# Kernel tuning notes

Measured on AMD Instinct MI355X. Metric: run time of the kernel, lower is better.

Reference implementation:

```python
import jax, jax.numpy as jnp
import numpy as np
from jax import lax

D_MODEL = 1024
D_IN = 1024        # expand=1 -> d_inner = d_model
N_STATE = 16       # d_state
DT_RANK = 64       # ceil(d_model/16)
D_FFN = 4096
BATCH, SEQ = 2, 2048


def setup_inputs() -> dict:
    key = jax.random.key(0)
    ks = jax.random.split(key, 12)
    r = lambda i, shape, s=0.02: jax.random.normal(ks[i], shape, jnp.float32) * s
    ones = lambda n: jnp.ones((n,), jnp.float32)
    zeros = lambda n: jnp.zeros((n,), jnp.float32)
    # S4D-real init for A
    A_log = jnp.log(jnp.tile(jnp.arange(1, N_STATE + 1, dtype=jnp.float32), (D_IN, 1)))
    return {
        "src": jax.random.normal(ks[0], (BATCH, SEQ, D_MODEL), jnp.float32),
        "in_proj_w": r(1, (2 * D_IN, D_MODEL)),
        "conv_w": r(2, (D_IN, 2), 0.5),
        "conv_b": zeros(D_IN),
        "x_proj_w": r(3, (DT_RANK + 2 * N_STATE, D_IN)),
        "dt_proj_w": r(4, (D_IN, DT_RANK), 0.1),
        "dt_proj_b": r(5, (D_IN,), 0.1),
        "A_log": A_log,
        "Dp": ones(D_IN),
        "out_proj_w": r(6, (D_MODEL, D_IN)),
        "mnorm_g": ones(D_MODEL), "mnorm_b": zeros(D_MODEL),
        "n1_g": ones(D_MODEL), "n1_b": zeros(D_MODEL),
        "n2_g": ones(D_MODEL), "n2_b": zeros(D_MODEL),
        "n3_g": ones(D_MODEL), "n3_b": zeros(D_MODEL),
        "ffn_w1": r(7, (D_FFN, D_MODEL)),
        "ffn_w2": r(8, (D_MODEL, D_FFN)),
        "fe_w": r(9, (D_MODEL, D_MODEL)),
        "fe_b": zeros(D_MODEL),
    }


def _ln(x, g, b, eps=1e-5):
    m = x.mean(-1, keepdims=True)
    v = ((x - m) ** 2).mean(-1, keepdims=True)
    return (x - m) / jnp.sqrt(v + eps) * g + b


def _mamba(x, in_proj_w, conv_w, conv_b, x_proj_w, dt_proj_w, dt_proj_b,
           A_log, Dp, out_proj_w):
    B, L, _ = x.shape
    xz = x @ in_proj_w.T                       # (B,L,2*D_IN)
    x_in, z = jnp.split(xz, 2, axis=-1)
    # depthwise causal conv1d, kernel size 2: y[l] = w0*x[l-1] + w1*x[l] + b
    x_prev = jnp.pad(x_in, ((0, 0), (1, 0), (0, 0)))[:, :L]
    x_c = jax.nn.silu(x_prev * conv_w[:, 0] + x_in * conv_w[:, 1] + conv_b)
    x_dbl = x_c @ x_proj_w.T                   # (B,L,DT_RANK+2N)
    dt, Bm, Cm = jnp.split(x_dbl, [DT_RANK, DT_RANK + N_STATE], axis=-1)
    delta = jax.nn.softplus(dt @ dt_proj_w.T + dt_proj_b)   # (B,L,D_IN)
    A = -jnp.exp(A_log)                        # (D_IN,N)
    deltaA = jnp.exp(delta[..., None] * A)                   # (B,L,D_IN,N)
    dBu = delta[..., None] * Bm[:, :, None, :] * x_c[..., None]

    def step(h, t):
        dA_t, dBu_t, C_t = t                   # (B,D_IN,N),(B,D_IN,N),(B,N)
        h = dA_t * h + dBu_t
        y = jnp.einsum('bdn,bn->bd', h, C_t)
        return h, y

    h0 = jnp.zeros((B, D_IN, N_STATE), x.dtype)
    _, ys = lax.scan(step, h0,
                     (deltaA.transpose(1, 0, 2, 3),
                      dBu.transpose(1, 0, 2, 3),
                      Cm.transpose(1, 0, 2)))
    y = ys.transpose(1, 0, 2)                  # (B,L,D_IN)
    y = (y + x_c * Dp) * jax.nn.silu(z)
    return y @ out_proj_w.T


def reference(src, in_proj_w, conv_w, conv_b, x_proj_w, dt_proj_w, dt_proj_b,
              A_log, Dp, out_proj_w, mnorm_g, mnorm_b, n1_g, n1_b, n2_g, n2_b,
              n3_g, n3_b, ffn_w1, ffn_w2, fe_w, fe_b):
    # src1 = MambaBlock(norm1(src)); dropout = identity (eval)
    h = _mamba(_ln(src, n1_g, n1_b), in_proj_w, conv_w, conv_b, x_proj_w,
               dt_proj_w, dt_proj_b, A_log, Dp, out_proj_w)
    src = src + _ln(h, mnorm_g, mnorm_b)
    # FFN: Linear -> LeakyReLU(0.01) -> Linear (no bias)
    f = _ln(src, n2_g, n2_b) @ ffn_w1.T
    f = jnp.where(f >= 0, f, 0.01 * f) @ ffn_w2.T
    src = src + f
    src = src + (_ln(src, n3_g, n3_b) @ fe_w.T + fe_b)
    return src
```

## Files before the change

### kernel.cpp

```cpp
#include <hip/hip_runtime.h>
#include <hip/hip_bf16.h>
#include <cstddef>

#define L_SEQ   2048
#define NBATCH  2
#define NROWS   (NBATCH * L_SEQ)
#define NSTATE  16
#define CH      64
#define NCHUNK  (L_SEQ / CH)

typedef __bf16 bf16x8 __attribute__((ext_vector_type(8)));
typedef float  f32x4  __attribute__((ext_vector_type(4)));
typedef unsigned short u16x4 __attribute__((ext_vector_type(4)));

static __device__ __forceinline__ unsigned short f2bf(float f) {
  unsigned int x = __builtin_bit_cast(unsigned int, f);
  x += 0x7fffu + ((x >> 16) & 1u);
  return (unsigned short)(x >> 16);
}
static __device__ __forceinline__ float bf2f(unsigned short u) {
  return __builtin_bit_cast(float, ((unsigned int)u) << 16);
}

#define GLDS(g, l) __builtin_amdgcn_global_load_lds( \
    (const __attribute__((address_space(1))) void*)(g), \
    (__attribute__((address_space(3))) void*)(l), 16, 0, 0)

#define DRAIN_VM() asm volatile("s_waitcnt vmcnt(0)" ::: "memory")

__global__ __launch_bounds__(256) void cvt_bf16_kernel(
    const float* __restrict__ in, unsigned short* __restrict__ out, int n4)
{
  const int i = blockIdx.x * 256 + threadIdx.x;
  if (i < n4) {
    const float4 v = reinterpret_cast<const float4*>(in)[i];
    u16x4 o;
    o[0] = f2bf(v.x); o[1] = f2bf(v.y); o[2] = f2bf(v.z); o[3] = f2bf(v.w);
    reinterpret_cast<u16x4*>(out)[i] = o;
  }
}

__global__ __launch_bounds__(256) void cvt_all_kernel(
    const float* __restrict__ ipw, const float* __restrict__ xpw,
    const float* __restrict__ dtw, const float* __restrict__ opw,
    const float* __restrict__ w1,  const float* __restrict__ w2,
    const float* __restrict__ few,
    unsigned short* __restrict__ o_ipw, unsigned short* __restrict__ o_xpw,
    unsigned short* __restrict__ o_dtw, unsigned short* __restrict__ o_opw,
    unsigned short* __restrict__ o_w1,  unsigned short* __restrict__ o_w2,
    unsigned short* __restrict__ o_few)
{
  int i = blockIdx.x * 256 + threadIdx.x;
  const float* src; unsigned short* dst;
  if (i < 524288)                 { src = ipw; dst = o_ipw; }
  else if ((i -= 524288) < 24576) { src = xpw; dst = o_xpw; }
  else if ((i -= 24576) < 16384)  { src = dtw; dst = o_dtw; }
  else if ((i -= 16384) < 262144) { src = opw; dst = o_opw; }
  else if ((i -= 262144) < 1048576){ src = w1; dst = o_w1; }
  else if ((i -= 1048576) < 1048576){ src = w2; dst = o_w2; }
  else if ((i -= 1048576) < 262144){ src = few; dst = o_few; }
  else return;
  const float4 v = reinterpret_cast<const float4*>(src)[i];
  u16x4 o;
  o[0] = f2bf(v.x); o[1] = f2bf(v.y); o[2] = f2bf(v.z); o[3] = f2bf(v.w);
  reinterpret_cast<u16x4*>(dst)[i] = o;
}

__global__ __launch_bounds__(256) void ln_kernel(
    const float* __restrict__ in, const float* __restrict__ g,
    const float* __restrict__ bta, const float* __restrict__ res,
    float* __restrict__ out, unsigned short* __restrict__ outb)
{
  const int row = blockIdx.x;
  const int tid = threadIdx.x;
  __shared__ float sm[8];
  const float4 v = reinterpret_cast<const float4*>(in + (size_t)row * 1024)[tid];
  float s = v.x + v.y + v.z + v.w;
#pragma unroll
  for (int o = 32; o > 0; o >>= 1) s += __shfl_down(s, o, 64);
  if ((tid & 63) == 0) sm[tid >> 6] = s;
  __syncthreads();
  const float mean = (sm[0] + sm[1] + sm[2] + sm[3]) * (1.f / 1024.f);
  const float dx = v.x - mean, dy = v.y - mean, dz = v.z - mean, dw = v.w - mean;
  float q = dx * dx + dy * dy + dz * dz + dw * dw;
#pragma unroll
  for (int o = 32; o > 0; o >>= 1) q += __shfl_down(q, o, 64);
  __syncthreads();
  if ((tid & 63) == 0) sm[tid >> 6] = q;
  __syncthreads();
  const float var = (sm[0] + sm[1] + sm[2] + sm[3]) * (1.f / 1024.f);
  const float rstd = rsqrtf(var + 1e-5f);
  const float4 gv = reinterpret_cast<const float4*>(g)[tid];
  const float4 bv = reinterpret_cast<const float4*>(bta)[tid];
  float4 o4;
  o4.x = dx * rstd * gv.x + bv.x;
  o4.y = dy * rstd * gv.y + bv.y;
  o4.z = dz * rstd * gv.z + bv.z;
  o4.w = dw * rstd * gv.w + bv.w;
  if (outb) {
    u16x4 ob;
    ob[0] = f2bf(o4.x); ob[1] = f2bf(o4.y); ob[2] = f2bf(o4.z); ob[3] = f2bf(o4.w);
    reinterpret_cast<u16x4*>(outb + (size_t)row * 1024)[tid] = ob;
  } else {
    if (res) {
      const float4 rv = reinterpret_cast<const float4*>(res + (size_t)row * 1024)[tid];
      o4.x += rv.x; o4.y += rv.y; o4.z += rv.z; o4.w += rv.w;
    }
    reinterpret_cast<float4*>(out + (size_t)row * 1024)[tid] = o4;
  }
}

__global__ __launch_bounds__(256) void gemm_bf16_kernel(
    const unsigned short* __restrict__ A, int lda,
    const unsigned short* __restrict__ B, int ldb,
    void* __restrict__ Cv, int ldc,
    const float* __restrict__ bias, const float* __restrict__ res,
    int K, int act, int outbf, int gy)
{
  __shared__ unsigned short As[2][128 * 32];
  __shared__ unsigned short Bs[2][128 * 32];
  const int t = threadIdx.x;
  const int w = t >> 6, l = t & 63;

  const int q = gridDim.x >> 3;
  const int nid = (blockIdx.x & 7) * q + (blockIdx.x >> 3);
  const int bm = (nid / gy) * 128;
  const int bn = (nid % gy) * 128;

  const int wr = (w >> 1) * 64, wc = (w & 1) * 64;
  f32x4 acc[4][4] = {};

  const int srow = t >> 2;
  const int sk = (t & 3) * 8;
  const unsigned short* gA0 = A + (size_t)(bm + srow) * lda + sk;
  const unsigned short* gA1 = gA0 + (size_t)64 * lda;
  const unsigned short* gB0 = B + (size_t)(bn + srow) * ldb + sk;
  const unsigned short* gB1 = gB0 + (size_t)64 * ldb;

  const int fr = l & 15;
  const int kb = (l >> 4) * 8;

#define STAGE(buf, k0) do { \
    GLDS(gA0 + (k0), &As[buf][w * 512]); \
    GLDS(gA1 + (k0), &As[buf][2048 + w * 512]); \
    GLDS(gB0 + (k0), &Bs[buf][w * 512]); \
    GLDS(gB1 + (k0), &Bs[buf][2048 + w * 512]); \
  } while (0)

#define COMPUTE(buf) do { \
    bf16x8 af[4], bfr[4]; \
    _Pragma("unroll") \
    for (int i = 0; i < 4; ++i) \
      af[i] = *reinterpret_cast<const bf16x8*>(&As[buf][(wr + i * 16 + fr) * 32 + kb]); \
    _Pragma("unroll") \
    for (int j = 0; j < 4; ++j) \
      bfr[j] = *reinterpret_cast<const bf16x8*>(&Bs[buf][(wc + j * 16 + fr) * 32 + kb]); \
    _Pragma("unroll") \
    for (int i = 0; i < 4; ++i) \
      _Pragma("unroll") \
      for (int j = 0; j < 4; ++j) \
        acc[i][j] = __builtin_amdgcn_mfma_f32_16x16x32_bf16(af[i], bfr[j], acc[i][j], 0, 0, 0); \
  } while (0)

  STAGE(0, 0);
  DRAIN_VM();
  __syncthreads();
  int cur = 0;
  for (int k0 = 32; k0 < K; k0 += 32) {
    __builtin_amdgcn_sched_barrier(0);
    STAGE(cur ^ 1, k0);
    __builtin_amdgcn_sched_barrier(0);
    COMPUTE(cur);
    DRAIN_VM();
    __syncthreads();
    cur ^= 1;
  }
  COMPUTE(cur);
#undef STAGE
#undef COMPUTE

  const int crow = (l >> 4) * 4;
  const int ccol = l & 15;
  float* Cf = (float*)Cv;
  unsigned short* Cb = (unsigned short*)Cv;
#pragma unroll
  for (int i = 0; i < 4; ++i) {
#pragma unroll
    for (int j = 0; j < 4; ++j) {
      const int n = bn + wc + j * 16 + ccol;
      const float bv = bias ? bias[n] : 0.f;
#pragma unroll
      for (int r = 0; r < 4; ++r) {
        const int m = bm + wr + i * 16 + crow + r;
        float v = acc[i][j][r] + bv;
        if (act == 1) v = (v > 20.f) ? v : __logf(1.f + __expf(v));
        else if (act == 2) v = (v >= 0.f) ? v : 0.01f * v;
        if (res) v += res[(size_t)m * ldc + n];
        if (outbf) Cb[(size_t)m * ldc + n] = f2bf(v);
        else       Cf[(size_t)m * ldc + n] = v;
      }
    }
  }
}

__global__ __launch_bounds__(512) void gemm256_kernel(
    const unsigned short* __restrict__ A, int lda,
    const unsigned short* __restrict__ B, int ldb,
    void* __restrict__ Cv, int ldc,
    const float* __restrict__ bias, const float* __restrict__ res,
    int K, int act, int outbf, int gy)
{
  __shared__ __align__(16) unsigned char smem[131072];
  const int t = threadIdx.x;
  const int w = t >> 6, l = t & 63;

  const int q = gridDim.x >> 3;
  const int nid = (blockIdx.x & 7) * q + (blockIdx.x >> 3);
  const int bm = (nid / gy) * 256;
  const int bn = (nid % gy) * 256;

  const int wr = (w >> 2) * 128;
  const int wc = (w & 3) * 64;
  f32x4 acc[8][4] = {};

  const int srow = t >> 3;
  const int sk8 = (t & 7) * 8;
  const unsigned short* gA = A + (size_t)(bm + srow) * lda + sk8;
  const unsigned short* gB = B + (size_t)(bn + srow) * ldb + sk8;

  const int fr = l & 15;
  const int kb = (l >> 4) * 8;

#define SA6(buf) (smem + (buf) * 32768)
#define SB6(buf) (smem + 65536 + (buf) * 32768)

#define STAGE6(buf, k0) do { \
    _Pragma("unroll") \
    for (int ii = 0; ii < 4; ++ii) { \
      GLDS(gA + (k0) + (size_t)(ii * 64) * lda, SA6(buf) + ii * 8192 + w * 1024); \
      GLDS(gB + (k0) + (size_t)(ii * 64) * ldb, SB6(buf) + ii * 8192 + w * 1024); \
    } \
  } while (0)

#define COMPUTE6(buf) do { \
    _Pragma("unroll") \
    for (int s = 0; s < 2; ++s) { \
      bf16x8 af[8], bfr[4]; \
      _Pragma("unroll") \
      for (int j = 0; j < 4; ++j) \
        bfr[j] = *reinterpret_cast<const bf16x8*>((const unsigned short*)SB6(buf) + (wc + j * 16 + fr) * 64 + s * 32 + kb); \
      _Pragma("unroll") \
      for (int i = 0; i < 8; ++i) \
        af[i] = *reinterpret_cast<const bf16x8*>((const unsigned short*)SA6(buf) + (wr + i * 16 + fr) * 64 + s * 32 + kb); \
      _Pragma("unroll") \
      for (int i = 0; i < 8; ++i) \
        _Pragma("unroll") \
        for (int j = 0; j < 4; ++j) \
          acc[i][j] = __builtin_amdgcn_mfma_f32_16x16x32_bf16(af[i], bfr[j], acc[i][j], 0, 0, 0); \
    } \
  } while (0)

  STAGE6(0, 0);
  DRAIN_VM();
  __syncthreads();
  int cur = 0;
  for (int k0 = 64; k0 < K; k0 += 64) {
    __builtin_amdgcn_sched_barrier(0);
    STAGE6(cur ^ 1, k0);
    __builtin_amdgcn_sched_barrier(0);
    COMPUTE6(cur);
    DRAIN_VM();
    __syncthreads();
    cur ^= 1;
  }
  COMPUTE6(cur);
#undef STAGE6
#undef COMPUTE6
#undef SA6
#undef SB6

  const int crow = (l >> 4) * 4;
  const int ccol = l & 15;
  float* Cf = (float*)Cv;
  unsigned short* Cb = (unsigned short*)Cv;
#pragma unroll
  for (int i = 0; i < 8; ++i) {
#pragma unroll
    for (int j = 0; j < 4; ++j) {
      const int n = bn + wc + j * 16 + ccol;
      const float bv = bias ? bias[n] : 0.f;
#pragma unroll
      for (int r = 0; r < 4; ++r) {
        const int m = bm + wr + i * 16 + crow + r;
        float v = acc[i][j][r] + bv;
        if (act == 1) v = (v > 20.f) ? v : __logf(1.f + __expf(v));
        else if (act == 2) v = (v >= 0.f) ? v : 0.01f * v;
        if (res) v += res[(size_t)m * ldc + n];
        if (outbf) Cb[(size_t)m * ldc + n] = f2bf(v);
        else       Cf[(size_t)m * ldc + n] = v;
      }
    }
  }
}

template<int BK>
__global__ __launch_bounds__(512) void gemm_ksplit_kernel(
    const unsigned short* __restrict__ A, int lda,
    const unsigned short* __restrict__ B, int ldb,
    void* __restrict__ Cv, int ldc,
    const float* __restrict__ bias, const float* __restrict__ res,
    int K, int act, int outbf, int gy)
{
  constexpr int ABYTES = 128 * BK * 2;
  constexpr int NISS = (BK == 32) ? 2 : 4;
  constexpr int RPI  = (BK == 32) ? 64 : 32;
  constexpr int NS   = BK / 32;
  __shared__ __align__(16) unsigned char smem[8 * ABYTES];
  const int tid = threadIdx.x;
  const int grp = tid >> 8;
  const int t = tid & 255;
  const int w = t >> 6, l = t & 63;

  const int q = gridDim.x >> 3;
  const int nid = (blockIdx.x & 7) * q + (blockIdx.x >> 3);
  const int bm = (nid / gy) * 128;
  const int bn = (nid % gy) * 128;

  const int K2 = K >> 1;
  const int koff = grp * K2;
  const int wr = (w >> 1) * 64, wc = (w & 1) * 64;
  f32x4 acc[4][4] = {};

  const int srow = (BK == 32) ? (t >> 2) : (t >> 3);
  const int sk   = (BK == 32) ? ((t & 3) * 8) : ((t & 7) * 8);
  const unsigned short* gA = A + (size_t)(bm + srow) * lda + koff + sk;
  const unsigned short* gB = B + (size_t)(bn + srow) * ldb + koff + sk;

  const int gbase = grp * 2 * ABYTES;
  const int fr = l & 15;
  const int kb = (l >> 4) * 8;

#define SAb(buf) (smem + gbase + (buf) * ABYTES)
#define SBb(buf) (smem + 4 * ABYTES + gbase + (buf) * ABYTES)

#define STAGEK(buf, k0) do { \
    _Pragma("unroll") \
    for (int ii = 0; ii < NISS; ++ii) { \
      GLDS(gA + (k0) + (size_t)ii * RPI * lda, SAb(buf) + ii * 4096 + w * 1024); \
      GLDS(gB + (k0) + (size_t)ii * RPI * ldb, SBb(buf) + ii * 4096 + w * 1024); \
    } \
  } while (0)

#define COMPUTEK(buf) do { \
    _Pragma("unroll") \
    for (int s = 0; s < NS; ++s) { \
      bf16x8 af[4], bfr[4]; \
      _Pragma("unroll") \
      for (int i = 0; i < 4; ++i) \
        af[i] = *reinterpret_cast<const bf16x8*>((const unsigned short*)SAb(buf) + (wr + i * 16 + fr) * BK + s * 32 + kb); \
      _Pragma("unroll") \
      for (int j = 0; j < 4; ++j) \
        bfr[j] = *reinterpret_cast<const bf16x8*>((const unsigned short*)SBb(buf) + (wc + j * 16 + fr) * BK + s * 32 + kb); \
      _Pragma("unroll") \
      for (int i = 0; i < 4; ++i) \
        _Pragma("unroll") \
        for (int j = 0; j < 4; ++j) \
          acc[i][j] = __builtin_amdgcn_mfma_f32_16x16x32_bf16(af[i], bfr[j], acc[i][j], 0, 0, 0); \
    } \
  } while (0)

  STAGEK(0, 0);
  DRAIN_VM();
  __syncthreads();
  int cur = 0;
  for (int k0 = BK; k0 < K2; k0 += BK) {
    __builtin_amdgcn_sched_barrier(0);
    STAGEK(cur ^ 1, k0);
    __builtin_amdgcn_sched_barrier(0);
    COMPUTEK(cur);
    DRAIN_VM();
    __syncthreads();
    cur ^= 1;
  }
  COMPUTEK(cur);
#undef STAGEK
#undef COMPUTEK
#undef SAb
#undef SBb

  __syncthreads();
  float* red = (float*)smem;
  if (grp) {
#pragma unroll
    for (int i = 0; i < 4; ++i)
#pragma unroll
      for (int j = 0; j < 4; ++j)
        *reinterpret_cast<f32x4*>(&red[(t << 6) + (i * 4 + j) * 4]) = acc[i][j];
  }
  __syncthreads();
  if (!grp) {
    const int crow = (l >> 4) * 4;
    const int ccol = l & 15;
    float* Cf = (float*)Cv;
    unsigned short* Cb = (unsigned short*)Cv;
#pragma unroll
    for (int i = 0; i < 4; ++i) {
#pragma unroll
      for (int j = 0; j < 4; ++j) {
        const f32x4 o = *reinterpret_cast<const f32x4*>(&red[(t << 6) + (i * 4 + j) * 4]);
        const int n = bn + wc + j * 16 + ccol;
        const float bv = bias ? bias[n] : 0.f;
#pragma unroll
        for (int r = 0; r < 4; ++r) {
          const int m = bm + wr + i * 16 + crow + r;
          float v = acc[i][j][r] + o[r] + bv;
          if (act == 1) v = (v > 20.f) ? v : __logf(1.f + __expf(v));
          else if (act == 2) v = (v >= 0.f) ? v : 0.01f * v;
          if (res) v += res[(size_t)m * ldc + n];
          if (outbf) Cb[(size_t)m * ldc + n] = f2bf(v);
          else       Cf[(size_t)m * ldc + n] = v;
        }
      }
    }
  }
}

__global__ __launch_bounds__(256) void xproj_kernel(
    const unsigned short* __restrict__ A, int lda,
    const unsigned short* __restrict__ B, int ldb,
    float* __restrict__ C)
{
  __shared__ unsigned short As[2][128 * 32];
  __shared__ unsigned short Bs[2][96 * 32];
  const int t = threadIdx.x;
  const int w = t >> 6, l = t & 63;
  const int bm = blockIdx.x * 128;
  const int kbase = blockIdx.y * 128;

  f32x4 acc[2][6] = {};

  const int srow = t >> 2;
  const int sk = (t & 3) * 8;
  const unsigned short* gA0 = A + (size_t)(bm + srow) * lda + kbase + sk;
  const unsigned short* gA1 = gA0 + (size_t)64 * lda;
  const unsigned short* gB0 = B + (size_t)srow * ldb + kbase + sk;
  const unsigned short* gB1 = gB0 + (size_t)64 * ldb;

  const int fr = l & 15;
  const int kb = (l >> 4) * 8;

#define STAGEX(buf, k0) do { \
    GLDS(gA0 + (k0), &As[buf][w * 512]); \
    GLDS(gA1 + (k0), &As[buf][2048 + w * 512]); \
    GLDS(gB0 + (k0), &Bs[buf][w * 512]); \
    if (w < 2) GLDS(gB1 + (k0), &Bs[buf][2048 + w * 512]); \
  } while (0)

#define COMPUTEX(buf) do { \
    bf16x8 af[2], bfr[6]; \
    _Pragma("unroll") \
    for (int i = 0; i < 2; ++i) \
      af[i] = *reinterpret_cast<const bf16x8*>(&As[buf][(w * 32 + i * 16 + fr) * 32 + kb]); \
    _Pragma("unroll") \
    for (int j = 0; j < 6; ++j) \
      bfr[j] = *reinterpret_cast<const bf16x8*>(&Bs[buf][(j * 16 + fr) * 32 + kb]); \
    _Pragma("unroll") \
    for (int i = 0; i < 2; ++i) \
      _Pragma("unroll") \
      for (int j = 0; j < 6; ++j) \
        acc[i][j] = __builtin_amdgcn_mfma_f32_16x16x32_bf16(af[i], bfr[j], acc[i][j], 0, 0, 0); \
  } while (0)

  STAGEX(0, 0);
  DRAIN_VM();
  __syncthreads();
  int cur = 0;
  for (int s = 1; s < 4; ++s) {
    __builtin_amdgcn_sched_barrier(0);
    STAGEX(cur ^ 1, s * 32);
    __builtin_amdgcn_sched_barrier(0);
    COMPUTEX(cur);
    DRAIN_VM();
    __syncthreads();
    cur ^= 1;
  }
  COMPUTEX(cur);
#undef STAGEX
#undef COMPUTEX

  const int crow = (l >> 4) * 4;
  const int ccol = l & 15;
#pragma unroll
  for (int i = 0; i < 2; ++i)
#pragma unroll
    for (int j = 0; j < 6; ++j)
#pragma unroll
      for (int r = 0; r < 4; ++r) {
        const int m = bm + w * 32 + i * 16 + crow + r;
        const int n = j * 16 + ccol;
        atomicAdd(&C[(size_t)m * 96 + n], acc[i][j][r]);
      }
}

__global__ __launch_bounds__(256) void conv_silu_kernel(
    const unsigned short* __restrict__ xz, const float* __restrict__ cw,
    const float* __restrict__ cb, float* __restrict__ xc,
    unsigned short* __restrict__ xcb)
{
  const int idx = blockIdx.x * 256 + threadIdx.x;
  const int row = idx >> 10;
  const int d = idx & 1023;
  const int l = row & (L_SEQ - 1);
  const float cur = bf2f(xz[(size_t)row * 2048 + d]);
  const float prev = (l == 0) ? 0.f : bf2f(xz[(size_t)(row - 1) * 2048 + d]);
  const float v = prev * cw[d * 2 + 0] + cur * cw[d * 2 + 1] + cb[d];
  const float sv = v / (1.f + __expf(-v));
  xc[idx] = sv;
  xcb[idx] = f2bf(sv);
}

__global__ __launch_bounds__(256) void scan_pass1(
    const float* __restrict__ delta, const float* __restrict__ xc,
    const float* __restrict__ xdbl, const float* __restrict__ A_log,
    float* __restrict__ hfin, float* __restrict__ pcum)
{
  const int tid = threadIdx.x;
  const int db = blockIdx.x & 3;
  const int c = (blockIdx.x >> 2) & (NCHUNK - 1);
  const int b = blockIdx.x >> 7;
  const int d = db * 256 + tid;
  __shared__ float Bsh[CH][16];
  {
    const int lr = tid >> 2, q = tid & 3;
    const float* p = xdbl + ((size_t)(b * L_SEQ + c * CH + lr) * 96) + 64 + q * 4;
    *reinterpret_cast<float4*>(&Bsh[lr][q * 4]) = *reinterpret_cast<const float4*>(p);
  }
  float a[NSTATE];
#pragma unroll
  for (int n = 0; n < NSTATE; ++n) a[n] = -__expf(A_log[d * 16 + n]);
  __syncthreads();
  float h[NSTATE], P[NSTATE];
#pragma unroll
  for (int n = 0; n < NSTATE; ++n) { h[n] = 0.f; P[n] = 1.f; }
  const size_t rowbase = (size_t)(b * L_SEQ + c * CH);
  for (int s = 0; s < CH; ++s) {
    const size_t row = rowbase + s;
    const float dl = delta[row * 1024 + d];
    const float xcv = xc[row * 1024 + d];
#pragma unroll
    for (int n = 0; n < NSTATE; ++n) {
      const float dA = __expf(dl * a[n]);
      h[n] = h[n] * dA + (dl * Bsh[s][n]) * xcv;
      P[n] *= dA;
    }
  }
  const size_t base = ((size_t)((b * NCHUNK + c) * 1024 + d)) * 16;
  float4* hp = reinterpret_cast<float4*>(hfin + base);
  float4* pp = reinterpret_cast<float4*>(pcum + base);
#pragma unroll
  for (int qq = 0; qq < 4; ++qq) {
    hp[qq] = make_float4(h[qq * 4], h[qq * 4 + 1], h[qq * 4 + 2], h[qq * 4 + 3]);
    pp[qq] = make_float4(P[qq * 4], P[qq * 4 + 1], P[qq * 4 + 2], P[qq * 4 + 3]);
  }
}

__global__ __launch_bounds__(256) void scan_pass2(
    const float* __restrict__ hfin, const float* __restrict__ pcum,
    float* __restrict__ hstart)
{
  const int t = blockIdx.x * 256 + threadIdx.x;
  const int b = t >> 14;
  const int dn = t & 16383;
  const size_t base = (size_t)b * NCHUNK * 16384 + dn;
  float h = 0.f;
  for (int c = 0; c < NCHUNK; ++c) {
    const size_t idx = base + (size_t)c * 16384;
    hstart[idx] = h;
    h = pcum[idx] * h + hfin[idx];
  }
}

__global__ __launch_bounds__(256) void scan_pass3(
    const float* __restrict__ delta, const float* __restrict__ xc,
    const float* __restrict__ xdbl, const float* __restrict__ A_log,
    const float* __restrict__ hstart, const float* __restrict__ Dp,
    const unsigned short* __restrict__ xz, unsigned short* __restrict__ yout)
{
  const int tid = threadIdx.x;
  const int db = blockIdx.x & 3;
  const int c = (blockIdx.x >> 2) & (NCHUNK - 1);
  const int b = blockIdx.x >> 7;
  const int d = db * 256 + tid;
  __shared__ float Bsh[CH][16];
  __shared__ float Csh[CH][16];
  {
    const int lr = tid >> 2, q = tid & 3;
    const float* p = xdbl + ((size_t)(b * L_SEQ + c * CH + lr) * 96);
    *reinterpret_cast<float4*>(&Bsh[lr][q * 4]) = *reinterpret_cast<const float4*>(p + 64 + q * 4);
    *reinterpret_cast<float4*>(&Csh[lr][q * 4]) = *reinterpret_cast<const float4*>(p + 80 + q * 4);
  }
  float a[NSTATE];
#pragma unroll
  for (int n = 0; n < NSTATE; ++n) a[n] = -__expf(A_log[d * 16 + n]);
  float h[NSTATE];
  {
    const size_t base = ((size_t)((b * NCHUNK + c) * 1024 + d)) * 16;
    const float4* hp = reinterpret_cast<const float4*>(hstart + base);
#pragma unroll
    for (int qq = 0; qq < 4; ++qq) {
      const float4 v = hp[qq];
      h[qq * 4] = v.x; h[qq * 4 + 1] = v.y; h[qq * 4 + 2] = v.z; h[qq * 4 + 3] = v.w;
    }
  }
  const float dpv = Dp[d];
  __syncthreads();
  const size_t rowbase = (size_t)(b * L_SEQ + c * CH);
  for (int s = 0; s < CH; ++s) {
    const size_t row = rowbase + s;
    const float dl = delta[row * 1024 + d];
    const float xcv = xc[row * 1024 + d];
    float y = 0.f;
#pragma unroll
    for (int n = 0; n < NSTATE; ++n) {
      const float dA = __expf(dl * a[n]);
      h[n] = h[n] * dA + (dl * Bsh[s][n]) * xcv;
      y += h[n] * Csh[s][n];
    }
    const float z = bf2f(xz[row * 2048 + 1024 + d]);
    const float sil = z / (1.f + __expf(-z));
    yout[row * 1024 + d] = f2bf((y + xcv * dpv) * sil);
  }
}

extern "C" void kernel_launch(void* const* d_in, const int* in_sizes, int n_in,
                              void* d_out, int out_size, void* d_ws, size_t ws_size,
                              hipStream_t stream)
{
  (void)in_sizes; (void)n_in; (void)out_size; (void)ws_size;
  const float* src        = (const float*)d_in[0];
  const float* in_proj_w  = (const float*)d_in[1];
  const float* conv_w     = (const float*)d_in[2];
  const float* conv_b     = (const float*)d_in[3];
  const float* x_proj_w   = (const float*)d_in[4];
  const float* dt_proj_w  = (const float*)d_in[5];
  const float* dt_proj_b  = (const float*)d_in[6];
  const float* A_log      = (const float*)d_in[7];
  const float* Dp         = (const float*)d_in[8];
  const float* out_proj_w = (const float*)d_in[9];
  const float* mnorm_g    = (const float*)d_in[10];
  const float* mnorm_b    = (const float*)d_in[11];
  const float* n1_g       = (const float*)d_in[12];
  const float* n1_b       = (const float*)d_in[13];
  const float* n2_g       = (const float*)d_in[14];
  const float* n2_b       = (const float*)d_in[15];
  const float* n3_g       = (const float*)d_in[16];
  const float* n3_b       = (const float*)d_in[17];
  const float* ffn_w1     = (const float*)d_in[18];
  const float* ffn_w2     = (const float*)d_in[19];
  const float* fe_w       = (const float*)d_in[20];
  const float* fe_b       = (const float*)d_in[21];
  float* out = (float*)d_out;
  float* ws  = (float*)d_ws;

  unsigned short* xzb  = (unsigned short*)ws;
  unsigned short* xdblb= (unsigned short*)(ws + 4194304);
  unsigned short* dtwb = (unsigned short*)(ws + 4390912);
  float* xc    = ws + 8388608;
  float* xdbl  = ws + 12582912;
  float* delta = ws + 13107200;
  float* s5    = ws + 17301504;
  float* src1  = ws + 21495808;
  float* hfin  = ws + 25690112;
  float* pcum  = ws + 26738688;
  float* hst   = ws + 27787264;
  unsigned short* s1b  = (unsigned short*)(ws + 28835840);
  unsigned short* xcb  = (unsigned short*)(ws + 30932992);
  unsigned short* yb   = (unsigned short*)(ws + 33030144);
  unsigned short* f1b  = (unsigned short*)(ws + 35127296);
  unsigned short* ipwb = (unsigned short*)(ws + 43515904);
  unsigned short* xpwb = (unsigned short*)(ws + 44564480);
  unsigned short* opwb = (unsigned short*)(ws + 44613632);
  unsigned short* w1b  = (unsigned short*)(ws + 45137920);
  unsigned short* w2b  = (unsigned short*)(ws + 47235072);
  unsigned short* fewb = (unsigned short*)(ws + 49332224);

  const dim3 blk(256);
  const dim3 blk512(512);

  cvt_all_kernel<<<12448, blk, 0, stream>>>(
      in_proj_w, x_proj_w, dt_proj_w, out_proj_w, ffn_w1, ffn_w2, fe_w,
      ipwb, xpwb, dtwb, opwb, w1b, w2b, fewb);

  ln_kernel<<<NROWS, blk, 0, stream>>>(src, n1_g, n1_b, nullptr, nullptr, s1b);
  gemm_ksplit_kernel<32><<<512, blk512, 0, stream>>>(s1b, 1024, ipwb, 1024, xzb, 2048,
                                                     nullptr, nullptr, 1024, 0, 1, 16);
  conv_silu_kernel<<<16384, blk, 0, stream>>>(xzb, conv_w, conv_b, xc, xcb);
  hipMemsetAsync(xdbl, 0, (size_t)NROWS * 96 * sizeof(float), stream);
  xproj_kernel<<<dim3(32, 8), blk, 0, stream>>>(xcb, 1024, xpwb, 1024, xdbl);
  cvt_bf16_kernel<<<384, blk, 0, stream>>>(xdbl, xdblb, 98304);
  gemm_bf16_kernel<<<256, blk, 0, stream>>>(xdblb, 96, dtwb, 64, delta, 1024,
                                            dt_proj_b, nullptr, 64, 1, 0, 8);
  scan_pass1<<<256, blk, 0, stream>>>(delta, xc, xdbl, A_log, hfin, pcum);
  scan_pass2<<<128, blk, 0, stream>>>(hfin, pcum, hst);
  scan_pass3<<<256, blk, 0, stream>>>(delta, xc, xdbl, A_log, hst, Dp, xzb, yb);
  gemm_ksplit_kernel<64><<<256, blk512, 0, stream>>>(yb, 1024, opwb, 1024, s5, 1024,
                                                     nullptr, nullptr, 1024, 0, 0, 8);
  ln_kernel<<<NROWS, blk, 0, stream>>>(s5, mnorm_g, mnorm_b, src, src1, nullptr);
  ln_kernel<<<NROWS, blk, 0, stream>>>(src1, n2_g, n2_b, nullptr, nullptr, s1b);
  gemm256_kernel<<<256, blk512, 0, stream>>>(s1b, 1024, w1b, 1024, f1b, 4096,
                                             nullptr, nullptr, 1024, 2, 1, 16);
  gemm_ksplit_kernel<64><<<256, blk512, 0, stream>>>(f1b, 4096, w2b, 4096, s5, 1024,
                                                     nullptr, src1, 4096, 0, 0, 8);
  ln_kernel<<<NROWS, blk, 0, stream>>>(s5, n3_g, n3_b, nullptr, nullptr, s1b);
  gemm_ksplit_kernel<64><<<256, blk512, 0, stream>>>(s1b, 1024, fewb, 1024, out, 1024,
                                                     fe_b, s5, 1024, 0, 0, 8);
}
```

Measured before the change: 397.5 us.

## Restructure GEMM main loop into 4-stage K=32 pipeline with two tiles in flight

```diff
diff --git a/kernel.cpp b/kernel.cpp
--- a/kernel.cpp
+++ b/kernel.cpp
@@ -223,61 +223,59 @@
   const int wc = (w & 3) * 64;
   f32x4 acc[8][4] = {};
 
-  const int srow = t >> 3;
-  const int sk8 = (t & 7) * 8;
-  const unsigned short* gA = A + (size_t)(bm + srow) * lda + sk8;
-  const unsigned short* gB = B + (size_t)(bn + srow) * ldb + sk8;
+  const int srow = t >> 2;
+  const int sk = (t & 3) * 8;
+  const unsigned short* gA = A + (size_t)(bm + srow) * lda + sk;
+  const unsigned short* gB = B + (size_t)(bn + srow) * ldb + sk;
 
   const int fr = l & 15;
   const int kb = (l >> 4) * 8;
 
-#define SA6(buf) (smem + (buf) * 32768)
-#define SB6(buf) (smem + 65536 + (buf) * 32768)
-
-#define STAGE6(buf, k0) do { \
-    _Pragma("unroll") \
-    for (int ii = 0; ii < 4; ++ii) { \
-      GLDS(gA + (k0) + (size_t)(ii * 64) * lda, SA6(buf) + ii * 8192 + w * 1024); \
-      GLDS(gB + (k0) + (size_t)(ii * 64) * ldb, SB6(buf) + ii * 8192 + w * 1024); \
-    } \
+#define SA7(s) (smem + (s) * 16384)
+#define SB7(s) (smem + 65536 + (s) * 16384)
+
+#define STAGE7(s, k0) do { \
+    GLDS(gA + (k0), SA7(s) + w * 1024); \
+    GLDS(gA + (k0) + (size_t)128 * lda, SA7(s) + 8192 + w * 1024); \
+    GLDS(gB + (k0), SB7(s) + w * 1024); \
+    GLDS(gB + (k0) + (size_t)128 * ldb, SB7(s) + 8192 + w * 1024); \
   } while (0)
 
-#define COMPUTE6(buf) do { \
-    _Pragma("unroll") \
-    for (int s = 0; s < 2; ++s) { \
-      bf16x8 af[8], bfr[4]; \
+#define COMPUTE7(s) do { \
+    bf16x8 af[8], bfr[4]; \
+    _Pragma("unroll") \
+    for (int j = 0; j < 4; ++j) \
+      bfr[j] = *reinterpret_cast<const bf16x8*>((const unsigned short*)SB7(s) + (wc + j * 16 + fr) * 32 + kb); \
+    _Pragma("unroll") \
+    for (int i = 0; i < 8; ++i) \
+      af[i] = *reinterpret_cast<const bf16x8*>((const unsigned short*)SA7(s) + (wr + i * 16 + fr) * 32 + kb); \
+    _Pragma("unroll") \
+    for (int i = 0; i < 8; ++i) \
       _Pragma("unroll") \
       for (int j = 0; j < 4; ++j) \
-        bfr[j] = *reinterpret_cast<const bf16x8*>((const unsigned short*)SB6(buf) + (wc + j * 16 + fr) * 64 + s * 32 + kb); \
-      _Pragma("unroll") \
-      for (int i = 0; i < 8; ++i) \
-        af[i] = *reinterpret_cast<const bf16x8*>((const unsigned short*)SA6(buf) + (wr + i * 16 + fr) * 64 + s * 32 + kb); \
-      _Pragma("unroll") \
-      for (int i = 0; i < 8; ++i) \
-        _Pragma("unroll") \
-        for (int j = 0; j < 4; ++j) \
-          acc[i][j] = __builtin_amdgcn_mfma_f32_16x16x32_bf16(af[i], bfr[j], acc[i][j], 0, 0, 0); \
-    } \
+        acc[i][j] = __builtin_amdgcn_mfma_f32_16x16x32_bf16(af[i], bfr[j], acc[i][j], 0, 0, 0); \
   } while (0)
 
-  STAGE6(0, 0);
-  DRAIN_VM();
-  __syncthreads();
-  int cur = 0;
-  for (int k0 = 64; k0 < K; k0 += 64) {
-    __builtin_amdgcn_sched_barrier(0);
-    STAGE6(cur ^ 1, k0);
-    __builtin_amdgcn_sched_barrier(0);
-    COMPUTE6(cur);
-    DRAIN_VM();
-    __syncthreads();
-    cur ^= 1;
-  }
-  COMPUTE6(cur);
-#undef STAGE6
-#undef COMPUTE6
-#undef SA6
-#undef SB6
+  const int nt = K >> 5;
+  STAGE7(0, 0);
+  if (nt > 1) STAGE7(1, 32);
+  asm volatile("s_waitcnt vmcnt(4)" ::: "memory");
+  __builtin_amdgcn_s_barrier();
+  for (int kt = 0; kt < nt; ++kt) {
+    const int s = kt & 3;
+    __builtin_amdgcn_sched_barrier(0);
+    if (kt + 2 < nt) STAGE7((kt + 2) & 3, (kt + 2) * 32);
+    __builtin_amdgcn_sched_barrier(0);
+    COMPUTE7(s);
+    __builtin_amdgcn_sched_barrier(0);
+    if (kt + 2 < nt)      asm volatile("s_waitcnt vmcnt(4)" ::: "memory");
+    else if (kt + 1 < nt) asm volatile("s_waitcnt vmcnt(0)" ::: "memory");
+    __builtin_amdgcn_s_barrier();
+  }
+#undef STAGE7
+#undef COMPUTE7
+#undef SA7
+#undef SB7
 
   const int crow = (l >> 4) * 4;
   const int ccol = l & 15;
```

Result: no change. 401.7 us (+1.0%).

## Add 4-way intra-block K-split GEMM with 1024 threads for N=1024 GEMMs

Applied to the files above, without the earlier changes.

```diff
diff --git a/kernel.cpp b/kernel.cpp
--- a/kernel.cpp
+++ b/kernel.cpp
@@ -399,6 +399,137 @@
   }
   __syncthreads();
   if (!grp) {
+    const int crow = (l >> 4) * 4;
+    const int ccol = l & 15;
+    float* Cf = (float*)Cv;
+    unsigned short* Cb = (unsigned short*)Cv;
+#pragma unroll
+    for (int i = 0; i < 4; ++i) {
+#pragma unroll
+      for (int j = 0; j < 4; ++j) {
+        const f32x4 o = *reinterpret_cast<const f32x4*>(&red[(t << 6) + (i * 4 + j) * 4]);
+        const int n = bn + wc + j * 16 + ccol;
+        const float bv = bias ? bias[n] : 0.f;
+#pragma unroll
+        for (int r = 0; r < 4; ++r) {
+          const int m = bm + wr + i * 16 + crow + r;
+          float v = acc[i][j][r] + o[r] + bv;
+          if (act == 1) v = (v > 20.f) ? v : __logf(1.f + __expf(v));
+          else if (act == 2) v = (v >= 0.f) ? v : 0.01f * v;
+          if (res) v += res[(size_t)m * ldc + n];
+          if (outbf) Cb[(size_t)m * ldc + n] = f2bf(v);
+          else       Cf[(size_t)m * ldc + n] = v;
+        }
+      }
+    }
+  }
+}
+
+__global__ __launch_bounds__(1024) void gemm_ksplit4_kernel(
+    const unsigned short* __restrict__ A, int lda,
+    const unsigned short* __restrict__ B, int ldb,
+    void* __restrict__ Cv, int ldc,
+    const float* __restrict__ bias, const float* __restrict__ res,
+    int K, int act, int outbf, int gy)
+{
+  __shared__ __align__(16) unsigned char smem[131072];
+  const int tid = threadIdx.x;
+  const int grp = tid >> 8;
+  const int t = tid & 255;
+  const int w = t >> 6, l = t & 63;
+
+  const int q = gridDim.x >> 3;
+  const int nid = (blockIdx.x & 7) * q + (blockIdx.x >> 3);
+  const int bm = (nid / gy) * 128;
+  const int bn = (nid % gy) * 128;
+
+  const int K4 = K >> 2;
+  const int koff = grp * K4;
+  const int wr = (w >> 1) * 64, wc = (w & 1) * 64;
+  f32x4 acc[4][4] = {};
+
+  const int srow = t >> 2;
+  const int sk = (t & 3) * 8;
+  const unsigned short* gA = A + (size_t)(bm + srow) * lda + koff + sk;
+  const unsigned short* gB = B + (size_t)(bn + srow) * ldb + koff + sk;
+
+  const int gbase = grp * 16384;
+  const int fr = l & 15;
+  const int kb = (l >> 4) * 8;
+
+#define SA4(buf) (smem + gbase + (buf) * 8192)
+#define SB4(buf) (smem + 65536 + gbase + (buf) * 8192)
+
+#define STAGE4(buf, k0) do { \
+    GLDS(gA + (k0), SA4(buf) + w * 1024); \
+    GLDS(gA + (k0) + (size_t)64 * lda, SA4(buf) + 4096 + w * 1024); \
+    GLDS(gB + (k0), SB4(buf) + w * 1024); \
+    GLDS(gB + (k0) + (size_t)64 * ldb, SB4(buf) + 4096 + w * 1024); \
+  } while (0)
+
+#define COMPUTE4(buf) do { \
+    bf16x8 af[4], bfr[4]; \
+    _Pragma("unroll") \
+    for (int i = 0; i < 4; ++i) \
+      af[i] = *reinterpret_cast<const bf16x8*>((const unsigned short*)SA4(buf) + (wr + i * 16 + fr) * 32 + kb); \
+    _Pragma("unroll") \
+    for (int j = 0; j < 4; ++j) \
+      bfr[j] = *reinterpret_cast<const bf16x8*>((const unsigned short*)SB4(buf) + (wc + j * 16 + fr) * 32 + kb); \
+    _Pragma("unroll") \
+    for (int i = 0; i < 4; ++i) \
+      _Pragma("unroll") \
+      for (int j = 0; j < 4; ++j) \
+        acc[i][j] = __builtin_amdgcn_mfma_f32_16x16x32_bf16(af[i], bfr[j], acc[i][j], 0, 0, 0); \
+  } while (0)
+
+  STAGE4(0, 0);
+  DRAIN_VM();
+  __syncthreads();
+  int cur = 0;
+  for (int k0 = 32; k0 < K4; k0 += 32) {
+    __builtin_amdgcn_sched_barrier(0);
+    STAGE4(cur ^ 1, k0);
+    __builtin_amdgcn_sched_barrier(0);
+    COMPUTE4(cur);
+    DRAIN_VM();
+    __syncthreads();
+    cur ^= 1;
+  }
+  COMPUTE4(cur);
+#undef STAGE4
+#undef COMPUTE4
+#undef SA4
+#undef SB4
+
+  __syncthreads();
+  float* red = (float*)smem;
+  if (grp & 1) {
+    float* dst = red + ((grp >> 1) ? 16384 : 0);
+#pragma unroll
+    for (int i = 0; i < 4; ++i)
+#pragma unroll
+      for (int j = 0; j < 4; ++j)
+        *reinterpret_cast<f32x4*>(&dst[(t << 6) + (i * 4 + j) * 4]) = acc[i][j];
+  }
+  __syncthreads();
+  if (!(grp & 1)) {
+    const float* sp = red + ((grp >> 1) ? 16384 : 0);
+#pragma unroll
+    for (int i = 0; i < 4; ++i)
+#pragma unroll
+      for (int j = 0; j < 4; ++j)
+        acc[i][j] += *reinterpret_cast<const f32x4*>(&sp[(t << 6) + (i * 4 + j) * 4]);
+  }
+  __syncthreads();
+  if (grp == 2) {
+#pragma unroll
+    for (int i = 0; i < 4; ++i)
+#pragma unroll
+      for (int j = 0; j < 4; ++j)
+        *reinterpret_cast<f32x4*>(&red[(t << 6) + (i * 4 + j) * 4]) = acc[i][j];
+  }
+  __syncthreads();
+  if (grp == 0) {
     const int crow = (l >> 4) * 4;
     const int ccol = l & 15;
     float* Cf = (float*)Cv;
@@ -686,6 +817,7 @@
 
   const dim3 blk(256);
   const dim3 blk512(512);
+  const dim3 blk1024(1024);
 
   cvt_all_kernel<<<12448, blk, 0, stream>>>(
       in_proj_w, x_proj_w, dt_proj_w, out_proj_w, ffn_w1, ffn_w2, fe_w,
@@ -703,15 +835,15 @@
   scan_pass1<<<256, blk, 0, stream>>>(delta, xc, xdbl, A_log, hfin, pcum);
   scan_pass2<<<128, blk, 0, stream>>>(hfin, pcum, hst);
   scan_pass3<<<256, blk, 0, stream>>>(delta, xc, xdbl, A_log, hst, Dp, xzb, yb);
-  gemm_ksplit_kernel<64><<<256, blk512, 0, stream>>>(yb, 1024, opwb, 1024, s5, 1024,
-                                                     nullptr, nullptr, 1024, 0, 0, 8);
+  gemm_ksplit4_kernel<<<256, blk1024, 0, stream>>>(yb, 1024, opwb, 1024, s5, 1024,
+                                                   nullptr, nullptr, 1024, 0, 0, 8);
   ln_kernel<<<NROWS, blk, 0, stream>>>(s5, mnorm_g, mnorm_b, src, src1, nullptr);
   ln_kernel<<<NROWS, blk, 0, stream>>>(src1, n2_g, n2_b, nullptr, nullptr, s1b);
   gemm256_kernel<<<256, blk512, 0, stream>>>(s1b, 1024, w1b, 1024, f1b, 4096,
                                              nullptr, nullptr, 1024, 2, 1, 16);
-  gemm_ksplit_kernel<64><<<256, blk512, 0, stream>>>(f1b, 4096, w2b, 4096, s5, 1024,
-                                                     nullptr, src1, 4096, 0, 0, 8);
+  gemm_ksplit4_kernel<<<256, blk1024, 0, stream>>>(f1b, 4096, w2b, 4096, s5, 1024,
+                                                   nullptr, src1, 4096, 0, 0, 8);
   ln_kernel<<<NROWS, blk, 0, stream>>>(s5, n3_g, n3_b, nullptr, nullptr, s1b);
-  gemm_ksplit_kernel<64><<<256, blk512, 0, stream>>>(s1b, 1024, fewb, 1024, out, 1024,
-                                                     fe_b, s5, 1024, 0, 0, 8);
-}
+  gemm_ksplit4_kernel<<<256, blk1024, 0, stream>>>(s1b, 1024, fewb, 1024, out, 1024,
+                                                   fe_b, s5, 1024, 0, 0, 8);
+}
```

Measured after the change: 426.1 us. 1.07x slower.
